# Kernel optimization log

Measured on AMD Instinct MI355X. Metric: run time of the kernel, lower is better.

## Reference

```python
import jax, jax.numpy as jnp
import numpy as np

N_NODES = 100000
N_EDGES = 1600000
IN_DIM = 512
OUT_DIM = 64


def setup_inputs() -> dict:
    key = jax.random.key(0)
    k1, k2, k3 = jax.random.split(key, 3)
    x = jax.random.normal(k1, (N_NODES, IN_DIM), dtype=jnp.float32)
    edge_index = jax.random.randint(k2, (2, N_EDGES), 0, N_NODES, dtype=jnp.int64)
    # Glorot-ish init for the GCNConv linear weight, stored as [in, out]
    W = jax.random.normal(k3, (IN_DIM, OUT_DIM), dtype=jnp.float32) * (1.0 / np.sqrt(IN_DIM))
    b = jnp.zeros((OUT_DIM,), dtype=jnp.float32)
    return {"x": x, "edge_index": edge_index, "W": W, "b": b}


def reference(x, edge_index, W, b):
    N = x.shape[0]
    # --- gcn_norm: add self-loops, symmetric degree normalization ---
    loop = jnp.arange(N, dtype=edge_index.dtype)
    src = jnp.concatenate([edge_index[0], loop])  # message sources
    dst = jnp.concatenate([edge_index[1], loop])  # aggregation targets
    deg = jax.ops.segment_sum(jnp.ones_like(dst, dtype=x.dtype), dst, num_segments=N)
    deg_inv_sqrt = jnp.where(deg > 0, jax.lax.rsqrt(jnp.maximum(deg, 1.0)), 0.0)
    norm = deg_inv_sqrt[src] * deg_inv_sqrt[dst]  # [E+N]
    # --- linear transform then gather-scale-scatter aggregation ---
    h = x @ W                                   # [N, out]
    msg = h[src] * norm[:, None]                # [E+N, out]
    out = jax.ops.segment_sum(msg, dst, num_segments=N) + b
    return jax.nn.log_softmax(out, axis=1)
```

## Files before the change

### kernel.cpp

```cpp
#include <hip/hip_runtime.h>
#include <math.h>

#define N_NODES 100000
#define N_EDGES 1600000
#define IN_DIM 512
#define OUT_DIM 64
#define NB 1024
#define NPB 128
#define CHUNK (N_EDGES / NPB)
#define N_BUCKETS_USED 782
#define N_TILES (N_NODES / 16)

typedef __attribute__((ext_vector_type(8))) short short8;
typedef __attribute__((ext_vector_type(4))) float float4v;

__device__ __forceinline__ unsigned short f2bf(float f) {
    unsigned int u = __float_as_uint(f);
    u += 0x7fffu + ((u >> 16) & 1u);
    return (unsigned short)(u >> 16);
}
__device__ __forceinline__ float bf2f(unsigned short s) {
    return __uint_as_float(((unsigned int)s) << 16);
}

__global__ __launch_bounds__(256) void k_hist1(const int* __restrict__ dst,
                                               int* __restrict__ blockHist) {
    __shared__ int hist[NB];
    const int t = threadIdx.x, b = blockIdx.x;
    for (int k = t; k < NB; k += 256) hist[k] = 0;
    __syncthreads();
    const int e0 = b * CHUNK;
    for (int i = t; i < CHUNK; i += 256)
        atomicAdd(&hist[dst[e0 + i] >> 7], 1);
    __syncthreads();
    for (int k = t; k < NB; k += 256) blockHist[b * NB + k] = hist[k];
}

__global__ __launch_bounds__(256) void k_offsets(const int* __restrict__ blockHist,
                                                 int* __restrict__ blockStart,
                                                 int* __restrict__ bucketBase) {
    __shared__ int colsum[NB];
    __shared__ int bbase[NB + 1];
    __shared__ int wtot[4];
    const int t = threadIdx.x, lane = t & 63, w = t >> 6;
    for (int k = t; k < NB; k += 256) {
        int s = 0;
        for (int b = 0; b < NPB; ++b) s += blockHist[b * NB + k];
        colsum[k] = s;
    }
    __syncthreads();
    int c0 = colsum[t * 4 + 0], c1 = colsum[t * 4 + 1];
    int c2 = colsum[t * 4 + 2], c3 = colsum[t * 4 + 3];
    int tsum = c0 + c1 + c2 + c3;
    int incl = tsum;
#pragma unroll
    for (int off = 1; off < 64; off <<= 1) {
        int u = __shfl_up(incl, off, 64);
        if (lane >= off) incl += u;
    }
    if (lane == 63) wtot[w] = incl;
    __syncthreads();
    int woff = 0;
#pragma unroll
    for (int k2 = 0; k2 < 4; ++k2) if (k2 < w) woff += wtot[k2];
    int excl = woff + incl - tsum;
    bbase[t * 4 + 0] = excl;
    bbase[t * 4 + 1] = excl + c0;
    bbase[t * 4 + 2] = excl + c0 + c1;
    bbase[t * 4 + 3] = excl + c0 + c1 + c2;
    if (t == 255) bbase[NB] = excl + tsum;
    __syncthreads();
    for (int k = t; k < NB + 1; k += 256) bucketBase[k] = bbase[k];
    for (int k = t; k < NB; k += 256) {
        int run = bbase[k];
        for (int b = 0; b < NPB; ++b) {
            blockStart[b * NB + k] = run;
            run += blockHist[b * NB + k];
        }
    }
}

__global__ __launch_bounds__(256) void k_partition(const int* __restrict__ dst,
                                                   const int* __restrict__ src,
                                                   const int* __restrict__ blockStart,
                                                   int* __restrict__ parts) {
    __shared__ int cursor[NB];
    const int t = threadIdx.x, b = blockIdx.x;
    for (int k = t; k < NB; k += 256) cursor[k] = blockStart[b * NB + k];
    __syncthreads();
    const int e0 = b * CHUNK;
    for (int i = t; i < CHUNK; i += 256) {
        int d = dst[e0 + i];
        int s = src[e0 + i];
        int k = d >> 7;
        int pos = atomicAdd(&cursor[k], 1);
        parts[pos] = ((d & 127) << 17) | s;
    }
}

__global__ __launch_bounds__(256) void k_bucket(const int* __restrict__ parts,
                                                const int* __restrict__ bucketBase,
                                                int* __restrict__ degi,
                                                int* __restrict__ row_ptr,
                                                int* __restrict__ csr) {
    __shared__ int cnt[128];
    __shared__ int cur[128];
    __shared__ int wtot[2];
    const int t = threadIdx.x, k = blockIdx.x;
    const int base = bucketBase[k];
    const int n    = bucketBase[k + 1] - base;
    if (t < 128) cnt[t] = 0;
    __syncthreads();
    for (int i = t; i < n; i += 256)
        atomicAdd(&cnt[parts[base + i] >> 17], 1);
    __syncthreads();
    int incl = 0, v = 0;
    if (t < 128) {
        int lane = t & 63;
        v = cnt[t];
        incl = v;
#pragma unroll
        for (int off = 1; off < 64; off <<= 1) {
            int u = __shfl_up(incl, off, 64);
            if (lane >= off) incl += u;
        }
        if (lane == 63) wtot[t >> 6] = incl;
    }
    __syncthreads();
    if (t < 128) {
        int excl = incl - v + ((t >> 6) ? wtot[0] : 0);
        cur[t] = excl;
        int node = k * 128 + t;
        if (node < N_NODES) {
            degi[node]    = v;
            row_ptr[node] = base + excl;
        }
    }
    __syncthreads();
    for (int i = t; i < n; i += 256) {
        int code = parts[base + i];
        int nl = code >> 17, s = code & 0x1FFFF;
        int pos = atomicAdd(&cur[nl], 1);
        csr[base + pos] = s;
    }
}

__global__ __launch_bounds__(256) void k_wswz(const float* __restrict__ W,
                                              unsigned short* __restrict__ Wswz) {
    int t = blockIdx.x * 256 + threadIdx.x;
    if (t < IN_DIM * OUT_DIM) {
        int k = t >> 6, n = t & 63;
        int kt = k >> 5, kin = k & 31;
        int quad = kin >> 3, j = kin & 7;
        int ct = n >> 4, l16 = n & 15;
        int lane = quad * 16 + l16;
        Wswz[(((kt * 4 + ct) * 64 + lane) * 8) + j] = f2bf(W[t]);
    }
}

__global__ __launch_bounds__(512, 2) void k_gemm(const float* __restrict__ x,
                                              const unsigned short* __restrict__ Wswz,
                                              const int* __restrict__ degi,
                                              unsigned short* __restrict__ h) {
    __shared__ short8 Wlds[64][64];
    const int t = threadIdx.x;
    {
        const float4v* s = (const float4v*)Wswz;
        float4v* d = (float4v*)Wlds;
        for (int i = t; i < 4096; i += 512) d[i] = s[i];
    }
    __syncthreads();

    const int lane = t & 63;
    const int quad = lane >> 4, l16 = lane & 15;
    const int gw = blockIdx.x * 8 + (t >> 6);
    const int nw = gridDim.x * 8;

    for (int tile = gw; tile < N_TILES; tile += nw) {
        const int r0 = tile * 16;
        const float* xrow = x + (size_t)(r0 + l16) * IN_DIM + quad * 8;
        short8 abf[16];
#pragma unroll
        for (int kt = 0; kt < 16; ++kt) {
            float4v lo = *(const float4v*)(xrow + kt * 32);
            float4v hi = *(const float4v*)(xrow + kt * 32 + 4);
            union { short8 s8; unsigned short us[8]; } af;
            af.us[0] = f2bf(lo.x); af.us[1] = f2bf(lo.y);
            af.us[2] = f2bf(lo.z); af.us[3] = f2bf(lo.w);
            af.us[4] = f2bf(hi.x); af.us[5] = f2bf(hi.y);
            af.us[6] = f2bf(hi.z); af.us[7] = f2bf(hi.w);
            abf[kt] = af.s8;
        }
        float4v acc[4] = {{0.f,0.f,0.f,0.f},{0.f,0.f,0.f,0.f},
                          {0.f,0.f,0.f,0.f},{0.f,0.f,0.f,0.f}};
#pragma unroll
        for (int kt = 0; kt < 16; ++kt) {
#pragma unroll
            for (int ct = 0; ct < 4; ++ct) {
                short8 bf = Wlds[kt * 4 + ct][lane];
                acc[ct] = __builtin_amdgcn_mfma_f32_16x16x32_bf16(abf[kt], bf, acc[ct], 0, 0, 0);
            }
        }
#pragma unroll
        for (int reg = 0; reg < 4; ++reg) {
            int orow = r0 + quad * 4 + reg;
            float dinv = rsqrtf((float)(degi[orow] + 1));
#pragma unroll
            for (int ct = 0; ct < 4; ++ct)
                h[(size_t)orow * OUT_DIM + ct * 16 + l16] = f2bf(acc[ct][reg] * dinv);
        }
    }
}

__global__ __launch_bounds__(256) void k_gather(const int* __restrict__ degi,
                                                const int* __restrict__ row_ptr,
                                                const int* __restrict__ csr,
                                                const unsigned short* __restrict__ h,
                                                const float* __restrict__ b,
                                                float* __restrict__ out) {
    int node = blockIdx.x * 4 + (threadIdx.x >> 6);
    int lane = threadIdx.x & 63;
    if (node >= N_NODES) return;
    int cnt  = __builtin_amdgcn_readfirstlane(degi[node]);
    int base = __builtin_amdgcn_readfirstlane(row_ptr[node]);

    float acc = bf2f(h[(size_t)node * OUT_DIM + lane]);
    int e = 0;
    for (; e + 8 <= cnt; e += 8) {
        int s0 = csr[base + e + 0], s1 = csr[base + e + 1];
        int s2 = csr[base + e + 2], s3 = csr[base + e + 3];
        int s4 = csr[base + e + 4], s5 = csr[base + e + 5];
        int s6 = csr[base + e + 6], s7 = csr[base + e + 7];
        float v0 = bf2f(h[(size_t)s0 * OUT_DIM + lane]);
        float v1 = bf2f(h[(size_t)s1 * OUT_DIM + lane]);
        float v2 = bf2f(h[(size_t)s2 * OUT_DIM + lane]);
        float v3 = bf2f(h[(size_t)s3 * OUT_DIM + lane]);
        float v4 = bf2f(h[(size_t)s4 * OUT_DIM + lane]);
        float v5 = bf2f(h[(size_t)s5 * OUT_DIM + lane]);
        float v6 = bf2f(h[(size_t)s6 * OUT_DIM + lane]);
        float v7 = bf2f(h[(size_t)s7 * OUT_DIM + lane]);
        acc += ((v0 + v1) + (v2 + v3)) + ((v4 + v5) + (v6 + v7));
    }
    for (; e < cnt; ++e)
        acc += bf2f(h[(size_t)csr[base + e] * OUT_DIM + lane]);

    float v = acc * rsqrtf((float)(cnt + 1)) + b[lane];
    float m = v;
#pragma unroll
    for (int off = 32; off > 0; off >>= 1) m = fmaxf(m, __shfl_xor(m, off, 64));
    float ex = expf(v - m);
    float s = ex;
#pragma unroll
    for (int off = 32; off > 0; off >>= 1) s += __shfl_xor(s, off, 64);
    out[(size_t)node * OUT_DIM + lane] = v - m - logf(s);
}

extern "C" void kernel_launch(void* const* d_in, const int* in_sizes, int n_in,
                              void* d_out, int out_size, void* d_ws, size_t ws_size,
                              hipStream_t stream) {
    const float* x  = (const float*)d_in[0];
    const int*   ei = (const int*)d_in[1];
    const float* W  = (const float*)d_in[2];
    const float* b  = (const float*)d_in[3];
    float* out = (float*)d_out;

    char* ws = (char*)d_ws;
    int*            degi       = (int*)(ws + 0);
    int*            row_ptr    = (int*)(ws + 400000);
    int*            blockHist  = (int*)(ws + 800000);
    int*            blockStart = (int*)(ws + 1324288);
    int*            bucketBase = (int*)(ws + 1848576);
    unsigned short* Wswz       = (unsigned short*)(ws + 1852928);
    unsigned short* h          = (unsigned short*)(ws + 1918464);
    int*            parts      = (int*)(ws + 14718464);
    int*            csr        = (int*)(ws + 21118464);

    const int* src = ei;
    const int* dst = ei + N_EDGES;

    k_hist1    <<<NPB, 256, 0, stream>>>(dst, blockHist);
    k_offsets  <<<1,   256, 0, stream>>>(blockHist, blockStart, bucketBase);
    k_partition<<<NPB, 256, 0, stream>>>(dst, src, blockStart, parts);
    k_bucket   <<<N_BUCKETS_USED, 256, 0, stream>>>(parts, bucketBase, degi, row_ptr, csr);
    k_wswz     <<<(IN_DIM * OUT_DIM + 255) / 256, 256, 0, stream>>>(W, Wswz);
    k_gemm     <<<512, 512, 0, stream>>>(x, Wswz, degi, h);
    k_gather   <<<(N_NODES + 3) / 4, 256, 0, stream>>>(degi, row_ptr, csr, h, b, out);
}
```

Measured before the change: 489.3 us.

## Split GEMM output columns across waves with W held in registers

Restructures the GEMM so each of four waves in a block computes a 16-column slice for a shared 16-row tile, holding its W slice in registers instead of LDS. It adds a register-level prefetch of the next x chunk and assigns contiguous tile ranges per block. The aim is to drop the LDS load and sync and cut register pressure, but each x row is now loaded by four waves, relying on cache to avoid quadrupled global traffic.

New measurement: 563.6 us. 15.2% more time.

```diff
diff --git a/kernel.cpp b/kernel.cpp
--- a/kernel.cpp
+++ b/kernel.cpp
@@ -10,6 +10,7 @@
 #define CHUNK (N_EDGES / NPB)
 #define N_BUCKETS_USED 782
 #define N_TILES (N_NODES / 16)
+#define GEMM_BLOCKS 1024
 
 typedef __attribute__((ext_vector_type(8))) short short8;
 typedef __attribute__((ext_vector_type(4))) float float4v;
@@ -21,6 +22,14 @@
 }
 __device__ __forceinline__ float bf2f(unsigned short s) {
     return __uint_as_float(((unsigned int)s) << 16);
+}
+__device__ __forceinline__ short8 cvt8(float4v lo, float4v hi) {
+    union { short8 s8; unsigned short us[8]; } af;
+    af.us[0] = f2bf(lo.x); af.us[1] = f2bf(lo.y);
+    af.us[2] = f2bf(lo.z); af.us[3] = f2bf(lo.w);
+    af.us[4] = f2bf(hi.x); af.us[5] = f2bf(hi.y);
+    af.us[6] = f2bf(hi.z); af.us[7] = f2bf(hi.w);
+    return af.s8;
 }
 
 __global__ __launch_bounds__(256) void k_hist1(const int* __restrict__ dst,
@@ -158,56 +167,56 @@
     }
 }
 
-__global__ __launch_bounds__(512, 2) void k_gemm(const float* __restrict__ x,
+__global__ __launch_bounds__(256, 4) void k_gemm(const float* __restrict__ x,
                                               const unsigned short* __restrict__ Wswz,
                                               const int* __restrict__ degi,
                                               unsigned short* __restrict__ h) {
-    __shared__ short8 Wlds[64][64];
     const int t = threadIdx.x;
-    {
-        const float4v* s = (const float4v*)Wswz;
-        float4v* d = (float4v*)Wlds;
-        for (int i = t; i < 4096; i += 512) d[i] = s[i];
-    }
-    __syncthreads();
-
     const int lane = t & 63;
+    const int ct = t >> 6;
     const int quad = lane >> 4, l16 = lane & 15;
-    const int gw = blockIdx.x * 8 + (t >> 6);
-    const int nw = gridDim.x * 8;
-
-    for (int tile = gw; tile < N_TILES; tile += nw) {
+
+    short8 Wreg[16];
+#pragma unroll
+    for (int kt = 0; kt < 16; ++kt)
+        Wreg[kt] = *(const short8*)(Wswz + (((kt * 4 + ct) * 64 + lane) * 8));
+
+    const int nb = gridDim.x;
+    const int t0 = (int)(((long)blockIdx.x * N_TILES) / nb);
+    const int t1 = (int)(((long)(blockIdx.x + 1) * N_TILES) / nb);
+
+    for (int tile = t0; tile < t1; ++tile) {
         const int r0 = tile * 16;
         const float* xrow = x + (size_t)(r0 + l16) * IN_DIM + quad * 8;
-        short8 abf[16];
-#pragma unroll
-        for (int kt = 0; kt < 16; ++kt) {
-            float4v lo = *(const float4v*)(xrow + kt * 32);
-            float4v hi = *(const float4v*)(xrow + kt * 32 + 4);
-            union { short8 s8; unsigned short us[8]; } af;
-            af.us[0] = f2bf(lo.x); af.us[1] = f2bf(lo.y);
-            af.us[2] = f2bf(lo.z); af.us[3] = f2bf(lo.w);
-            af.us[4] = f2bf(hi.x); af.us[5] = f2bf(hi.y);
-            af.us[6] = f2bf(hi.z); af.us[7] = f2bf(hi.w);
-            abf[kt] = af.s8;
-        }
-        float4v acc[4] = {{0.f,0.f,0.f,0.f},{0.f,0.f,0.f,0.f},
-                          {0.f,0.f,0.f,0.f},{0.f,0.f,0.f,0.f}};
-#pragma unroll
-        for (int kt = 0; kt < 16; ++kt) {
-#pragma unroll
-            for (int ct = 0; ct < 4; ++ct) {
-                short8 bf = Wlds[kt * 4 + ct][lane];
-                acc[ct] = __builtin_amdgcn_mfma_f32_16x16x32_bf16(abf[kt], bf, acc[ct], 0, 0, 0);
+
+        float4v plo[2], phi[2];
+#pragma unroll
+        for (int kt = 0; kt < 2; ++kt) {
+            plo[kt] = *(const float4v*)(xrow + kt * 32);
+            phi[kt] = *(const float4v*)(xrow + kt * 32 + 4);
+        }
+        float4v acc = {0.f, 0.f, 0.f, 0.f};
+
+#pragma unroll 1
+        for (int kp = 0; kp < 8; ++kp) {
+            short8 a0 = cvt8(plo[0], phi[0]);
+            short8 a1 = cvt8(plo[1], phi[1]);
+            if (kp < 7) {
+#pragma unroll
+                for (int kt = 0; kt < 2; ++kt) {
+                    plo[kt] = *(const float4v*)(xrow + (kp + 1) * 64 + kt * 32);
+                    phi[kt] = *(const float4v*)(xrow + (kp + 1) * 64 + kt * 32 + 4);
+                }
             }
-        }
+            acc = __builtin_amdgcn_mfma_f32_16x16x32_bf16(a0, Wreg[kp * 2 + 0], acc, 0, 0, 0);
+            acc = __builtin_amdgcn_mfma_f32_16x16x32_bf16(a1, Wreg[kp * 2 + 1], acc, 0, 0, 0);
+        }
+
 #pragma unroll
         for (int reg = 0; reg < 4; ++reg) {
             int orow = r0 + quad * 4 + reg;
             float dinv = rsqrtf((float)(degi[orow] + 1));
-#pragma unroll
-            for (int ct = 0; ct < 4; ++ct)
-                h[(size_t)orow * OUT_DIM + ct * 16 + l16] = f2bf(acc[ct][reg] * dinv);
+            h[(size_t)orow * OUT_DIM + ct * 16 + l16] = f2bf(acc[reg] * dinv);
         }
     }
 }
@@ -283,6 +292,6 @@
     k_partition<<<NPB, 256, 0, stream>>>(dst, src, blockStart, parts);
     k_bucket   <<<N_BUCKETS_USED, 256, 0, stream>>>(parts, bucketBase, degi, row_ptr, csr);
     k_wswz     <<<(IN_DIM * OUT_DIM + 255) / 256, 256, 0, stream>>>(W, Wswz);
-    k_gemm     <<<512, 512, 0, stream>>>(x, Wswz, degi, h);
+    k_gemm     <<<GEMM_BLOCKS, 256, 0, stream>>>(x, Wswz, degi, h);
     k_gather   <<<(N_NODES + 3) / 4, 256, 0, stream>>>(degi, row_ptr, csr, h, b, out);
 }
```
